# Performance work log

Hardware: AMD Instinct MI355X
Metric: run time of the kernel (lower is better)

Reference implementation:

```python
import jax, jax.numpy as jnp
import numpy as np

H = 32          # total heads
K = 8           # active heads per token
D = 128         # head_dim = embed_dim // active_heads
E = 1024        # embed_dim
S = 1024        # seq_len
MAX_SEQ = 8192
BASE = 10000.0
SCALE = D ** -0.5
LB_W = 0.01
ENT_W = 0.01


def _rope(v, cos, sin):
    # v: (T, D); cos/sin: (T, D)
    v1, v2 = v[:, : D // 2], v[:, D // 2:]
    rot = jnp.concatenate([-v2, v1], axis=-1)
    return v * cos + rot * sin


def setup_inputs() -> dict:
    key = jax.random.key(0)
    ks = jax.random.split(key, 6)
    x = jax.random.normal(ks[0], (1, S, E), jnp.float32)
    Wq = jax.random.normal(ks[1], (E, H * D), jnp.float32) * 0.02
    Wk = jax.random.normal(ks[2], (E, H * D), jnp.float32) * 0.02
    Wv = jax.random.normal(ks[3], (E, H * D), jnp.float32) * 0.02
    Wr = jax.random.normal(ks[4], (E, H), jnp.float32) * 0.02
    Wo = jax.random.normal(ks[5], (K * D, E), jnp.float32) * 0.02
    head_counts = jnp.zeros((1, H), jnp.int32)
    return {"x": x, "Wq": Wq, "Wk": Wk, "Wv": Wv, "Wr": Wr, "Wo": Wo,
            "head_counts": head_counts}


def reference(x, Wq, Wk, Wv, Wr, Wo, head_counts):
    # ---- routing (eval mode: no gumbel noise) ----
    logits = x @ Wr                                   # (1, S, H)
    soft_probs = jax.nn.softmax(logits, axis=-1)
    top_logits, head_idx = jax.lax.top_k(logits, K)   # (1, S, K)
    head_w = jax.nn.softmax(top_logits, axis=-1)      # (1, S, K)

    # ---- aux loss ----
    primary = head_idx[..., 0]                        # (1, S)
    one_hot_p = jax.nn.one_hot(primary, H, dtype=jnp.float32)
    f = one_hot_p.mean(axis=1)                        # (1, H)
    p = soft_probs.mean(axis=1)                       # (1, H)
    balance = H * (f * p).sum(axis=-1).mean()
    entropy = -(soft_probs * jnp.log(soft_probs + 1e-8)).sum(axis=-1)
    entropy_loss = -entropy.mean()
    z_loss = (jax.nn.logsumexp(logits, axis=-1) ** 2).mean() * 0.01
    aux_loss = LB_W * balance + ENT_W * entropy_loss + z_loss

    # ---- projections + per-token gather of selected heads ----
    q_all = (x @ Wq).reshape(1, S, H, D)
    k_all = (x @ Wk).reshape(1, S, H, D)
    v_all = (x @ Wv).reshape(1, S, H, D)
    gidx = head_idx[..., None]                        # (1, S, K, 1)
    q = jnp.take_along_axis(q_all, gidx, axis=2)[0].reshape(S * K, D)
    k = jnp.take_along_axis(k_all, gidx, axis=2)[0].reshape(S * K, D)
    v = jnp.take_along_axis(v_all, gidx, axis=2)[0].reshape(S * K, D)

    heads_flat = head_idx[0].reshape(S * K)           # (T,)

    # rank of each dispatched token within its head (exclusive prefix count)
    oh = jax.nn.one_hot(heads_flat, H, dtype=jnp.int32)   # (T, H)
    excl = jnp.cumsum(oh, axis=0) - oh
    rank = jnp.take_along_axis(excl, heads_flat[:, None], axis=1)[:, 0]
    positions = rank + head_counts[0, heads_flat]
    positions = jnp.clip(positions, 0, MAX_SEQ - 1)

    # ---- per-head RoPE with per-head position counters ----
    inv_freq = 1.0 / (BASE ** (jnp.arange(0, D, 2, dtype=jnp.float32) / D))
    freqs = positions.astype(jnp.float32)[:, None] * inv_freq[None, :]
    emb = jnp.concatenate([freqs, freqs], axis=-1)    # (T, D)
    cos, sin = jnp.cos(emb), jnp.sin(emb)
    q = _rope(q, cos, sin)
    k = _rope(k, cos, sin)

    # ---- block-diagonal-causal attention (same head, earlier dispatch order) ----
    idx = jnp.arange(S * K)
    mask = (heads_flat[:, None] == heads_flat[None, :]) & (idx[None, :] <= idx[:, None])
    scores = (q @ k.T) * SCALE                        # (T, T)
    scores = jnp.where(mask, scores, jnp.float32(-1e30))
    attn = jax.nn.softmax(scores, axis=-1)
    out = attn @ v                                    # (T, D)

    # ---- combine with routing weights + output projection ----
    out = out.reshape(S, K, D) * head_w[0][..., None]
    out = out.reshape(S, K * D) @ Wo                  # (S, E)
    output = out[None]                                # (1, S, E)

    updated_counts = head_counts + oh.sum(axis=0)[None]
    return output, updated_counts, aux_loss
```

## Files before the change

kernel.cpp:

```cpp
#include <hip/hip_runtime.h>
#include <math.h>

#define S 1024
#define E 1024
#define H 32
#define KSEL 8
#define D 128
#define HD 4096
#define SK 8192
#define MAXL 1024
#define CAP 9216
#define ATTN_SCALE 0.08838834764831845f
#define SSTR 36
#define PSTR 40

#define NROUTERB 1024
#define NCONV 832
#define NTAB 512

typedef _Float16 half8 __attribute__((ext_vector_type(8)));
typedef _Float16 half4 __attribute__((ext_vector_type(4)));
typedef float floatx16 __attribute__((ext_vector_type(16)));
typedef float f4 __attribute__((ext_vector_type(4)));

#define GLOAD_LDS16(gsrc, ldst) \
    __builtin_amdgcn_global_load_lds( \
        (const __attribute__((address_space(1))) void*)(gsrc), \
        (__attribute__((address_space(3))) void*)(ldst), 16, 0, 0)

__device__ __forceinline__ void head_prefix(const int* __restrict__ hlen, int h,
                                            int lane, int& len, int& hb, int& lenp)
{
    int hl = (lane < 32) ? hlen[lane] : 0;
    int hp = (hl + 31) & ~31;
    int pref = hp;
    #pragma unroll
    for (int off = 1; off < 32; off <<= 1) {
        int t = __shfl_up(pref, off, 64);
        if (lane >= off) pref += t;
    }
    int excl = pref - hp;
    hb   = __shfl(excl, h, 64);
    len  = __shfl(hl, h, 64);
    lenp = (len + 31) & ~31;
}

__global__ __launch_bounds__(256) void router_conv_kernel(
    const float* __restrict__ x, const float* __restrict__ Wr,
    int* __restrict__ head_idx, float* __restrict__ head_w,
    float* __restrict__ pbuf, float* __restrict__ entz,
    _Float16* __restrict__ xh,
    const float* __restrict__ Wq, const float* __restrict__ Wk,
    const float* __restrict__ Wv, const float* __restrict__ Wo,
    _Float16* __restrict__ Wqkt, _Float16* __restrict__ Wot,
    float2* __restrict__ tab)
{
    int bid = blockIdx.x, tid = threadIdx.x;
    __shared__ __align__(16) char smem[128 * 128 * 2];
    if (bid >= NROUTERB + NCONV) {
        int base = (bid - NROUTERB - NCONV) * 1024;
        #pragma unroll
        for (int j = 0; j < 4; ++j) {
            int idx = base + j * 256 + tid;
            int p = idx >> 6, d2 = idx & 63;
            float inv = exp2f((float)d2 * -0.20762050f);
            float ang = (float)p * inv;
            float sn, cs;
            sincosf(ang, &sn, &cs);
            tab[idx] = make_float2(cs, sn);
        }
        return;
    }
    if (bid >= NROUTERB) {
        _Float16* tl = (_Float16*)smem;
        int cb = bid - NROUTERB;
        int z, rem;
        if (cb < 768) { z = cb >> 8; rem = cb & 255; }
        else          { z = 3;       rem = cb - 768; }
        const float* W = (z == 0) ? Wq : (z == 1) ? Wk : (z == 2) ? Wv : Wo;
        _Float16* T = (z < 3) ? (Wqkt + (size_t)z * HD * E) : Wot;
        int C = (z < 3) ? HD : 1024;
        int nc = C >> 7;
        int c0 = (rem % nc) * 128;
        int r0 = (rem / nc) * 128;
        #pragma unroll
        for (int p = 0; p < 16; ++p) {
            int idx = p * 256 + tid;
            int rr = idx >> 5, cg = (idx & 31) * 4;
            f4 v = *(const f4*)&W[(size_t)(r0 + rr) * C + c0 + cg];
            half4 o;
            o.x = (_Float16)v.x; o.y = (_Float16)v.y;
            o.z = (_Float16)v.z; o.w = (_Float16)v.w;
            int sc = cg ^ (((rr >> 3) & 7) << 2);
            *(half4*)&tl[rr * 128 + sc] = o;
        }
        __syncthreads();
        #pragma unroll
        for (int p = 0; p < 8; ++p) {
            int chunk = p * 256 + tid;
            int cc = chunk >> 4, ch = chunk & 15;
            int cidx = cc ^ ((ch & 7) << 2);
            half8 o;
            #pragma unroll
            for (int j = 0; j < 8; ++j)
                o[j] = tl[(ch * 8 + j) * 128 + cidx];
            *(half8*)&T[(size_t)(c0 + cc) * 1024 + r0 + ch * 8] = o;
        }
        return;
    }
    int s = bid;
    int w = tid >> 6, lane = tid & 63;
    int h = lane & 31;
    int seg = w * 2 + (lane >> 5);
    float* partial = (float*)smem;
    const float* xr = x + (size_t)s * E + seg * 128;
    const float* wr = Wr + (size_t)(seg * 128) * H + h;
    float a0 = 0.f, a1 = 0.f, a2 = 0.f, a3 = 0.f;
    #pragma unroll 4
    for (int e = 0; e < 128; e += 4) {
        a0 += xr[e]     * wr[e * H];
        a1 += xr[e + 1] * wr[(e + 1) * H];
        a2 += xr[e + 2] * wr[(e + 2) * H];
        a3 += xr[e + 3] * wr[(e + 3) * H];
    }
    float acc = (a0 + a1) + (a2 + a3);
    acc += __shfl_xor(acc, 32, 64);
    if (lane < 32) partial[w * 32 + h] = acc;
    __syncthreads();
    float logit = partial[h] + partial[32 + h] + partial[64 + h] + partial[96 + h];
    if (w == 0) {
        float m = logit;
        #pragma unroll
        for (int off = 16; off; off >>= 1) m = fmaxf(m, __shfl_xor(m, off, 64));
        float ex = expf(logit - m);
        float Z = ex;
        #pragma unroll
        for (int off = 16; off; off >>= 1) Z += __shfl_xor(Z, off, 64);
        float p = ex / Z;
        float es = p * logf(p + 1e-8f);
        #pragma unroll
        for (int off = 16; off; off >>= 1) es += __shfl_xor(es, off, 64);
        float lse = m + logf(Z);
        float lv = logit;
        float tv[KSEL]; int ti[KSEL];
        #pragma unroll
        for (int j = 0; j < KSEL; ++j) {
            float bv = lv; int bi = h;
            #pragma unroll
            for (int off = 16; off; off >>= 1) {
                float ov = __shfl_xor(bv, off, 64);
                int oi = __shfl_xor(bi, off, 64);
                if (ov > bv || (ov == bv && oi < bi)) { bv = ov; bi = oi; }
            }
            tv[j] = bv; ti[j] = bi;
            if (h == bi) lv = -INFINITY;
        }
        float Z2 = 0.f;
        #pragma unroll
        for (int j = 0; j < KSEL; ++j) Z2 += expf(tv[j] - tv[0]);
        if (lane < 32) pbuf[s * 32 + lane] = p;
        if (lane == 0) {
            entz[s * 2]     = es;
            entz[s * 2 + 1] = lse * lse;
            #pragma unroll
            for (int j = 0; j < KSEL; ++j) {
                head_idx[s * KSEL + j] = ti[j];
                head_w[s * KSEL + j]   = expf(tv[j] - tv[0]) / Z2;
            }
        }
    }
    {
        int e = tid * 4;
        f4 v = *(const f4*)&x[(size_t)s * E + e];
        half4 o;
        o.x = (_Float16)v.x; o.y = (_Float16)v.y; o.z = (_Float16)v.z; o.w = (_Float16)v.w;
        *(half4*)&xh[(size_t)s * E + e] = o;
    }
}

__global__ __launch_bounds__(256) void scan_aux_kernel(
    const int* __restrict__ head_idx, const int* __restrict__ head_counts,
    int* __restrict__ order, int* __restrict__ hlen, float* __restrict__ out_counts,
    const float* __restrict__ pbuf, const float* __restrict__ entz,
    float* __restrict__ out_aux)
{
    int bid = blockIdx.x, tid = threadIdx.x;
    if (bid == H) {
        int hh = tid & 31, grp = tid >> 5;
        __shared__ float red[256], red2[256];
        __shared__ float psum[32];
        __shared__ int hist[32];
        if (tid < 32) hist[tid] = 0;
        float ps = 0.f;
        for (int s = grp; s < S; s += 8) ps += pbuf[s * 32 + hh];
        red[tid] = ps;
        float es = 0.f, zs = 0.f;
        for (int s = tid; s < S; s += 256) { es += entz[s * 2]; zs += entz[s * 2 + 1]; }
        red2[tid] = es;
        __syncthreads();
        if (grp == 0) {
            float v = 0.f;
            #pragma unroll
            for (int j = 0; j < 8; ++j) v += red[j * 32 + hh];
            psum[hh] = v;
        }
        __syncthreads();
        red[tid] = zs;
        for (int s = tid; s < S; s += 256)
            atomicAdd(&hist[head_idx[s * KSEL]], 1);
        __syncthreads();
        for (int stp = 128; stp; stp >>= 1) {
            if (tid < stp) { red[tid] += red[tid + stp]; red2[tid] += red2[tid + stp]; }
            __syncthreads();
        }
        if (tid == 0) {
            float bal = 0.f;
            for (int j = 0; j < H; ++j)
                bal += ((float)hist[j] / (float)S) * (psum[j] / (float)S);
            bal *= (float)H;
            float ent_loss = red2[0] / (float)S;
            float z = red[0] / (float)S * 0.01f;
            out_aux[0] = 0.01f * bal + 0.01f * ent_loss + z;
        }
        return;
    }
    int h = bid;
    int wave = tid >> 6, lane = tid & 63;
    __shared__ int wtot[4][4];
    int base = 0;
    int hc = head_counts[h];
    int v0 = head_idx[tid],       v1 = head_idx[256 + tid];
    int v2 = head_idx[512 + tid], v3 = head_idx[768 + tid];
    unsigned long long lt = (1ull << lane) - 1ull;
    for (int c0 = 0; c0 < SK; c0 += 1024) {
        int n0 = 0, n1 = 0, n2 = 0, n3 = 0;
        if (c0 + 1024 < SK) {
            n0 = head_idx[c0 + 1024 + tid]; n1 = head_idx[c0 + 1280 + tid];
            n2 = head_idx[c0 + 1536 + tid]; n3 = head_idx[c0 + 1792 + tid];
        }
        bool p0 = (v0 == h), p1 = (v1 == h), p2 = (v2 == h), p3 = (v3 == h);
        unsigned long long m0 = __ballot(p0), m1 = __ballot(p1);
        unsigned long long m2 = __ballot(p2), m3 = __ballot(p3);
        int w0 = __popcll(m0 & lt), w1 = __popcll(m1 & lt);
        int w2 = __popcll(m2 & lt), w3 = __popcll(m3 & lt);
        if (lane == 0) {
            wtot[0][wave] = __popcll(m0); wtot[1][wave] = __popcll(m1);
            wtot[2][wave] = __popcll(m2); wtot[3][wave] = __popcll(m3);
        }
        __syncthreads();
        int pw[4], T[4];
        #pragma unroll
        for (int i = 0; i < 4; ++i) {
            int pre = 0, tot = 0;
            #pragma unroll
            for (int w = 0; w < 4; ++w) {
                int tv = wtot[i][w];
                if (w < wave) pre += tv;
                tot += tv;
            }
            pw[i] = pre; T[i] = tot;
        }
        if (p0) order[h * MAXL + base + pw[0] + w0] = c0 + tid;
        if (p1) order[h * MAXL + base + T[0] + pw[1] + w1] = c0 + 256 + tid;
        if (p2) order[h * MAXL + base + T[0] + T[1] + pw[2] + w2] = c0 + 512 + tid;
        if (p3) order[h * MAXL + base + T[0] + T[1] + T[2] + pw[3] + w3] = c0 + 768 + tid;
        base += T[0] + T[1] + T[2] + T[3];
        __syncthreads();
        v0 = n0; v1 = n1; v2 = n2; v3 = n3;
    }
    if (tid == 0) {
        hlen[h] = base;
        out_counts[h] = (float)(hc + base);
    }
}

__global__ __launch_bounds__(256) void qkv_mfma(
    const _Float16* __restrict__ xh, const _Float16* __restrict__ Wt,
    const int* __restrict__ order, const int* __restrict__ hlen,
    const int* __restrict__ head_counts, const float2* __restrict__ tab,
    _Float16* __restrict__ qh, _Float16* __restrict__ kh, _Float16* __restrict__ vT)
{
    int xid = blockIdx.x;
    int qkv = xid >> 5, h = xid & 31;
    int rt = blockIdx.y;
    int tid = threadIdx.x, wave = tid >> 6, lane = tid & 63;
    int len, hb, lenp;
    head_prefix(hlen, h, lane, len, hb, lenp);
    int row0 = rt * 64;
    if (row0 >= len) return;
    int wm = wave >> 1, wn = wave & 1;
    int l32 = lane & 31, g = lane >> 5;

    __shared__ _Float16 Bs[2][128 * 64];

    int arow_g = row0 + wm * 32 + l32;
    int tok = (arow_g < len) ? (order[h * MAXL + arow_g] >> 3) : 0;
    const _Float16* aptr = xh + (size_t)tok * E;
    const _Float16* Wb = Wt + (size_t)((qkv * H + h) * D) * E;

    auto stageB = [&](int buf, int k0) {
        #pragma unroll
        for (int it = 0; it < 4; ++it) {
            int f = it * 256 + tid;
            int row = f >> 3, c = f & 7;
            int sc = c ^ (row & 7);
            const _Float16* src = Wb + (size_t)row * E + k0 + sc * 8;
            GLOAD_LDS16(src, &Bs[buf][f * 8]);
        }
    };

    floatx16 acc[2] = {};
    half8 a_cur[4], a_nxt[4];
    #pragma unroll
    for (int ks = 0; ks < 4; ++ks)
        a_cur[ks] = *(const half8*)(aptr + ks * 16 + g * 8);

    auto compute = [&](int buf, half8* a) {
        #pragma unroll
        for (int ks = 0; ks < 4; ++ks) {
            int wchunk = ks * 2 + g;
            #pragma unroll
            for (int nf = 0; nf < 2; ++nf) {
                int brow = wn * 64 + nf * 32 + l32;
                half8 bf = *(const half8*)&Bs[buf][brow * 64 + (wchunk ^ (brow & 7)) * 8];
                acc[nf] = __builtin_amdgcn_mfma_f32_32x32x16_f16(a[ks], bf, acc[nf], 0, 0, 0);
            }
        }
    };

    stageB(0, 0);
    __syncthreads();
    int buf = 0;
    for (int k0 = 64; k0 < E; k0 += 64) {
        stageB(buf ^ 1, k0);
        #pragma unroll
        for (int ks = 0; ks < 4; ++ks)
            a_nxt[ks] = *(const half8*)(aptr + k0 + ks * 16 + g * 8);
        compute(buf, a_cur);
        __syncthreads();
        buf ^= 1;
        #pragma unroll
        for (int ks = 0; ks < 4; ++ks) a_cur[ks] = a_nxt[ks];
    }
    compute(buf, a_cur);

    if (qkv < 2) {
        _Float16* dst = (qkv == 0) ? qh : kh;
        float* scr = (float*)&Bs[0][0];
        __syncthreads();
        #pragma unroll
        for (int nf = 0; nf < 2; ++nf) {
            int col = wn * 64 + nf * 32 + l32;
            #pragma unroll
            for (int reg = 0; reg < 16; ++reg) {
                int rl = wm * 32 + (reg & 3) + 8 * (reg >> 2) + 4 * g;
                scr[rl * 128 + col] = acc[nf][reg];
            }
        }
        __syncthreads();
        int hc = head_counts[h];
        #pragma unroll
        for (int pass = 0; pass < 16; ++pass) {
            int idx = pass * 256 + tid;
            int r = idx >> 6, d2 = idx & 63;
            int slot = row0 + r;
            if (slot < len) {
                float v1 = scr[r * 128 + d2], v2 = scr[r * 128 + 64 + d2];
                int p = slot + hc;
                p = p < 0 ? 0 : (p > 8191 ? 8191 : p);
                float2 tt = tab[p * 64 + d2];
                _Float16* dp = dst + ((size_t)hb + slot) * D;
                dp[d2]      = (_Float16)(v1 * tt.x - v2 * tt.y);
                dp[d2 + 64] = (_Float16)(v2 * tt.x + v1 * tt.y);
            }
        }
    } else {
        #pragma unroll
        for (int nf = 0; nf < 2; ++nf) {
            int col = wn * 64 + nf * 32 + l32;
            #pragma unroll
            for (int q4 = 0; q4 < 4; ++q4) {
                int slot0 = row0 + wm * 32 + 8 * q4 + 4 * g;
                _Float16* vp = vT + (size_t)hb * D + (size_t)col * lenp + slot0;
                if (slot0 + 3 < len) {
                    half4 o;
                    o.x = (_Float16)acc[nf][q4 * 4 + 0];
                    o.y = (_Float16)acc[nf][q4 * 4 + 1];
                    o.z = (_Float16)acc[nf][q4 * 4 + 2];
                    o.w = (_Float16)acc[nf][q4 * 4 + 3];
                    *(half4*)vp = o;
                } else {
                    #pragma unroll
                    for (int r2 = 0; r2 < 4; ++r2) {
                        int sl = slot0 + r2;
                        if (sl < len) vp[r2] = (_Float16)acc[nf][q4 * 4 + r2];
                        else if (sl < lenp) vp[r2] = (_Float16)0.f;
                    }
                }
            }
        }
    }
}

__global__ __launch_bounds__(128) void attn_mfma(
    const _Float16* __restrict__ qh, const _Float16* __restrict__ kh,
    const _Float16* __restrict__ vT,
    const int* __restrict__ order, const int* __restrict__ hlen,
    const float* __restrict__ head_w, _Float16* __restrict__ ao)
{
    int h = blockIdx.x >> 5, qt = blockIdx.x & 31;
    int tid = threadIdx.x;
    int w = tid >> 6, lane = tid & 63;
    int len, hb, lenp;
    head_prefix(hlen, h, lane, len, hb, lenp);
    int row0 = qt * 32;
    if (row0 >= len) return;
    int l32 = lane & 31, g = lane >> 5;
    int srow = lane >> 1, shalf = lane & 1;

    __shared__ float Sld[2][32 * SSTR];
    __shared__ _Float16 Pld[2][32 * PSTR];
    __shared__ float alphaLd[2][32];
    __shared__ float mlLd[32][4];
    __shared__ float facLd[32][3];
    __shared__ int flatLd[32];
    __shared__ float Obuf[32][128];

    if (tid < 32) {
        int r = row0 + tid;
        flatLd[tid] = (r < len) ? order[h * MAXL + r] : -1;
    }

    const _Float16* qrow = qh + ((size_t)hb + row0 + l32) * D;
    half8 qf[8];
    #pragma unroll
    for (int t = 0; t < 8; ++t) qf[t] = *(const half8*)(qrow + t * 16 + g * 8);

    floatx16 O[4] = {};
    float m_run = -INFINITY, l_run = 0.f;

    if (w <= qt) {
        half8 kf[8], kfn[8], vv[8];
        {
            const _Float16* krow = kh + ((size_t)hb + w * 32 + l32) * D;
            #pragma unroll
            for (int t = 0; t < 8; ++t) kf[t] = *(const half8*)(krow + t * 16 + g * 8);
        }
        for (int kt = w; kt <= qt; kt += 2) {
            int col0 = kt * 32;
            floatx16 Sc = {};
            #pragma unroll
            for (int t = 0; t < 8; ++t)
                Sc = __builtin_amdgcn_mfma_f32_32x32x16_f16(qf[t], kf[t], Sc, 0, 0, 0);
            #pragma unroll
            for (int nt = 0; nt < 4; ++nt) {
                const _Float16* vp = vT + (size_t)hb * D + (size_t)(nt * 32 + l32) * lenp + col0;
                vv[nt * 2]     = *(const half8*)(vp + g * 8);
                vv[nt * 2 + 1] = *(const half8*)(vp + 16 + g * 8);
            }
            if (kt + 2 <= qt) {
                const _Float16* krow = kh + ((size_t)hb + col0 + 64 + l32) * D;
                #pragma unroll
                for (int t = 0; t < 8; ++t) kfn[t] = *(const half8*)(krow + t * 16 + g * 8);
            }
            bool diag = (kt == qt);
            #pragma unroll
            for (int reg = 0; reg < 16; ++reg) {
                int row = (reg & 3) + 8 * (reg >> 2) + 4 * g;
                float s = Sc[reg] * ATTN_SCALE;
                if (diag && l32 > row) s = -1e30f;
                Sld[w][row * SSTR + l32] = s;
            }
            __builtin_amdgcn_wave_barrier();
            const float* sp = &Sld[w][srow * SSTR + shalf * 16];
            float va[16];
            *(f4*)(va)      = *(const f4*)(sp);
            *(f4*)(va + 4)  = *(const f4*)(sp + 4);
            *(f4*)(va + 8)  = *(const f4*)(sp + 8);
            *(f4*)(va + 12) = *(const f4*)(sp + 12);
            float mt_ = va[0];
            #pragma unroll
            for (int j = 1; j < 16; ++j) mt_ = fmaxf(mt_, va[j]);
            mt_ = fmaxf(mt_, __shfl_xor(mt_, 1, 64));
            float m_new = fmaxf(m_run, mt_);
            float alpha = __expf(m_run - m_new);
            float p[16], tsum = 0.f;
            #pragma unroll
            for (int j = 0; j < 16; ++j) { p[j] = __expf(va[j] - m_new); tsum += p[j]; }
            tsum += __shfl_xor(tsum, 1, 64);
            l_run = l_run * alpha + tsum;
            m_run = m_new;
            half8 ph0, ph1;
            #pragma unroll
            for (int j = 0; j < 8; ++j) { ph0[j] = (_Float16)p[j]; ph1[j] = (_Float16)p[j + 8]; }
            *(half8*)&Pld[w][srow * PSTR + shalf * 16]     = ph0;
            *(half8*)&Pld[w][srow * PSTR + shalf * 16 + 8] = ph1;
            if (shalf == 0) alphaLd[w][srow] = alpha;
            __builtin_amdgcn_wave_barrier();
            f4 al[4];
            #pragma unroll
            for (int qq = 0; qq < 4; ++qq) al[qq] = *(const f4*)&alphaLd[w][4 * g + 8 * qq];
            #pragma unroll
            for (int reg = 0; reg < 16; ++reg) {
                float av = al[reg >> 2][reg & 3];
                O[0][reg] *= av; O[1][reg] *= av; O[2][reg] *= av; O[3][reg] *= av;
            }
            half8 pf0 = *(const half8*)&Pld[w][l32 * PSTR + g * 8];
            half8 pf1 = *(const half8*)&Pld[w][l32 * PSTR + 16 + g * 8];
            #pragma unroll
            for (int nt = 0; nt < 4; ++nt) {
                O[nt] = __builtin_amdgcn_mfma_f32_32x32x16_f16(pf0, vv[nt * 2],     O[nt], 0, 0, 0);
                O[nt] = __builtin_amdgcn_mfma_f32_32x32x16_f16(pf1, vv[nt * 2 + 1], O[nt], 0, 0, 0);
            }
            __builtin_amdgcn_wave_barrier();
            #pragma unroll
            for (int t = 0; t < 8; ++t) kf[t] = kfn[t];
        }
    }
    if (shalf == 0) { mlLd[srow][w * 2] = m_run; mlLd[srow][w * 2 + 1] = l_run; }
    __syncthreads();
    if (tid < 32) {
        float m0 = mlLd[tid][0], l0 = mlLd[tid][1];
        float m1 = mlLd[tid][2], l1 = mlLd[tid][3];
        float ms = fmaxf(m0, m1);
        float f0 = __expf(m0 - ms), f1 = __expf(m1 - ms);
        float lt = f0 * l0 + f1 * l1;
        int flat = flatLd[tid];
        float hw = (flat >= 0) ? head_w[flat] : 0.f;
        facLd[tid][0] = f1;
        facLd[tid][1] = hw / lt;
        facLd[tid][2] = f0;
    }
    __syncthreads();
    if (w == 1) {
        #pragma unroll
        for (int nt = 0; nt < 4; ++nt) {
            int col = nt * 32 + l32;
            #pragma unroll
            for (int reg = 0; reg < 16; ++reg) {
                int row = (reg & 3) + 8 * (reg >> 2) + 4 * g;
                Obuf[row][col] = O[nt][reg] * facLd[row][0];
            }
        }
    }
    __syncthreads();
    if (w == 0) {
        #pragma unroll
        for (int nt = 0; nt < 4; ++nt) {
            int col = nt * 32 + l32;
            #pragma unroll
            for (int reg = 0; reg < 16; ++reg) {
                int row = (reg & 3) + 8 * (reg >> 2) + 4 * g;
                int flat = flatLd[row];
                if (flat >= 0) {
                    float val = (O[nt][reg] * facLd[row][2] + Obuf[row][col]) * facLd[row][1];
                    ao[(size_t)flat * D + col] = (_Float16)val;
                }
            }
        }
    }
}

__global__ __launch_bounds__(256) void out_mfma(
    const _Float16* __restrict__ A, const _Float16* __restrict__ Bt,
    float* __restrict__ C)
{
    int n0 = blockIdx.x * 64, m0 = blockIdx.y * 64;
    int tid = threadIdx.x, wave = tid >> 6, lane = tid & 63;
    int wm = wave >> 1, wn = wave & 1;
    int l32 = lane & 31, g = lane >> 5;

    __shared__ _Float16 Bs[2][64 * 64];

    const _Float16* aptr = A + (size_t)(m0 + wm * 32 + l32) * 1024;

    auto stageB = [&](int buf, int k0) {
        #pragma unroll
        for (int it = 0; it < 2; ++it) {
            int f = it * 256 + tid;
            int row = f >> 3, c = f & 7;
            int sc = c ^ (row & 7);
            GLOAD_LDS16(Bt + (size_t)(n0 + row) * 1024 + k0 + sc * 8, &Bs[buf][f * 8]);
        }
    };

    floatx16 acc = {};
    int brow = wn * 32 + l32;
    half8 a_cur[4], a_nxt[4];
    #pragma unroll
    for (int ks = 0; ks < 4; ++ks)
        a_cur[ks] = *(const half8*)(aptr + ks * 16 + g * 8);

    auto compute = [&](int buf, half8* a) {
        #pragma unroll
        for (int ks = 0; ks < 4; ++ks) {
            int wchunk = ks * 2 + g;
            half8 bf = *(const half8*)&Bs[buf][brow * 64 + (wchunk ^ (brow & 7)) * 8];
            acc = __builtin_amdgcn_mfma_f32_32x32x16_f16(a[ks], bf, acc, 0, 0, 0);
        }
    };

    stageB(0, 0);
    __syncthreads();
    int buf = 0;
    for (int k0 = 64; k0 < 1024; k0 += 64) {
        stageB(buf ^ 1, k0);
        #pragma unroll
        for (int ks = 0; ks < 4; ++ks)
            a_nxt[ks] = *(const half8*)(aptr + k0 + ks * 16 + g * 8);
        compute(buf, a_cur);
        __syncthreads();
        buf ^= 1;
        #pragma unroll
        for (int ks = 0; ks < 4; ++ks) a_cur[ks] = a_nxt[ks];
    }
    compute(buf, a_cur);

    int col = n0 + wn * 32 + l32;
    #pragma unroll
    for (int reg = 0; reg < 16; ++reg) {
        int row = m0 + wm * 32 + (reg & 3) + 8 * (reg >> 2) + 4 * g;
        C[(size_t)row * 1024 + col] = acc[reg];
    }
}

extern "C" void kernel_launch(void* const* d_in, const int* in_sizes, int n_in,
                              void* d_out, int out_size, void* d_ws, size_t ws_size,
                              hipStream_t stream)
{
    const float* x  = (const float*)d_in[0];
    const float* Wq = (const float*)d_in[1];
    const float* Wk = (const float*)d_in[2];
    const float* Wv = (const float*)d_in[3];
    const float* Wr = (const float*)d_in[4];
    const float* Wo = (const float*)d_in[5];
    const int* head_counts = (const int*)d_in[6];
    float* out = (float*)d_out;

    float* head_w = (float*)d_ws;
    float* pbuf   = head_w + SK;
    float* entz   = pbuf + S * 32;
    int* head_idx = (int*)(entz + S * 2);
    int* order    = head_idx + SK;
    int* hlen     = order + H * MAXL;
    _Float16* xh   = (_Float16*)(hlen + 64);
    _Float16* aoh  = xh + (size_t)S * E;
    _Float16* Wqkt = aoh + (size_t)SK * D;
    _Float16* Wot  = Wqkt + (size_t)3 * HD * E;
    _Float16* qh   = Wot + (size_t)1024 * 1024;
    _Float16* kh   = qh + (size_t)CAP * D;
    _Float16* vT   = kh + (size_t)CAP * D;
    float2* tab    = (float2*)(vT + (size_t)CAP * D);

    router_conv_kernel<<<NROUTERB + NCONV + NTAB, 256, 0, stream>>>(
        x, Wr, head_idx, head_w, pbuf, entz, xh, Wq, Wk, Wv, Wo, Wqkt, Wot, tab);
    scan_aux_kernel<<<33, 256, 0, stream>>>(head_idx, head_counts, order, hlen,
                                            out + (size_t)S * E, pbuf, entz,
                                            out + (size_t)S * E + H);
    qkv_mfma<<<dim3(96, 16), 256, 0, stream>>>(xh, Wqkt, order, hlen, head_counts, tab,
                                               qh, kh, vT);
    attn_mfma<<<H * 32, 128, 0, stream>>>(qh, kh, vT, order, hlen, head_w, aoh);
    out_mfma<<<dim3(16, 16), 256, 0, stream>>>(aoh, Wot, out);
}
```

Baseline: 217.0 us.

## Fuse scan into router kernel, tile Q/K/V layouts, reverse attention tile order

Three independent changes. First, the scan/aux kernel is merged into the router/convert kernel: scan blocks spin on a global atomic counter until all router blocks have finished, which removes one kernel launch but adds a hipMemsetAsync and relies on the router blocks being scheduled before the scan blocks. Second, Q, K and V^T are written by the QKV kernel in a 32-row tiled, fragment-interleaved layout so the attention kernel's MFMA operand loads are contiguous per lane. Third, attention query tiles are issued in reverse order so the longest causal tiles start first, improving load balance.

```diff
diff --git a/kernel.cpp b/kernel.cpp
--- a/kernel.cpp
+++ b/kernel.cpp
@@ -15,6 +15,7 @@
 #define PSTR 40
 
 #define NROUTERB 1024
+#define NSCAN 33
 #define NCONV 832
 #define NTAB 512
 
@@ -27,6 +28,7 @@
     __builtin_amdgcn_global_load_lds( \
         (const __attribute__((address_space(1))) void*)(gsrc), \
         (__attribute__((address_space(3))) void*)(ldst), 16, 0, 0)
+
 
 __device__ __forceinline__ void head_prefix(const int* __restrict__ hlen, int h,
                                             int lane, int& len, int& hb, int& lenp)
@@ -53,27 +55,190 @@
     const float* __restrict__ Wq, const float* __restrict__ Wk,
     const float* __restrict__ Wv, const float* __restrict__ Wo,
     _Float16* __restrict__ Wqkt, _Float16* __restrict__ Wot,
-    float2* __restrict__ tab)
+    float2* __restrict__ tab,
+    const int* __restrict__ head_counts,
+    int* __restrict__ order, int* __restrict__ hlen,
+    float* __restrict__ out_counts, float* __restrict__ out_aux,
+    int* __restrict__ syncb)
 {
     int bid = blockIdx.x, tid = threadIdx.x;
     __shared__ __align__(16) char smem[128 * 128 * 2];
-    if (bid >= NROUTERB + NCONV) {
-        int base = (bid - NROUTERB - NCONV) * 1024;
-        #pragma unroll
-        for (int j = 0; j < 4; ++j) {
-            int idx = base + j * 256 + tid;
-            int p = idx >> 6, d2 = idx & 63;
-            float inv = exp2f((float)d2 * -0.20762050f);
-            float ang = (float)p * inv;
-            float sn, cs;
-            sincosf(ang, &sn, &cs);
-            tab[idx] = make_float2(cs, sn);
-        }
+    if (bid < NROUTERB) {
+        int s = bid;
+        int w = tid >> 6, lane = tid & 63;
+        int h = lane & 31;
+        int seg = w * 2 + (lane >> 5);
+        float* partial = (float*)smem;
+        const float* xr = x + (size_t)s * E + seg * 128;
+        const float* wr = Wr + (size_t)(seg * 128) * H + h;
+        float a0 = 0.f, a1 = 0.f, a2 = 0.f, a3 = 0.f;
+        #pragma unroll 4
+        for (int e = 0; e < 128; e += 4) {
+            a0 += xr[e]     * wr[e * H];
+            a1 += xr[e + 1] * wr[(e + 1) * H];
+            a2 += xr[e + 2] * wr[(e + 2) * H];
+            a3 += xr[e + 3] * wr[(e + 3) * H];
+        }
+        float acc = (a0 + a1) + (a2 + a3);
+        acc += __shfl_xor(acc, 32, 64);
+        if (lane < 32) partial[w * 32 + h] = acc;
+        __syncthreads();
+        float logit = partial[h] + partial[32 + h] + partial[64 + h] + partial[96 + h];
+        if (w == 0) {
+            float m = logit;
+            #pragma unroll
+            for (int off = 16; off; off >>= 1) m = fmaxf(m, __shfl_xor(m, off, 64));
+            float ex = expf(logit - m);
+            float Z = ex;
+            #pragma unroll
+            for (int off = 16; off; off >>= 1) Z += __shfl_xor(Z, off, 64);
+            float p = ex / Z;
+            float es = p * logf(p + 1e-8f);
+            #pragma unroll
+            for (int off = 16; off; off >>= 1) es += __shfl_xor(es, off, 64);
+            float lse = m + logf(Z);
+            float lv = logit;
+            float tv[KSEL]; int ti[KSEL];
+            #pragma unroll
+            for (int j = 0; j < KSEL; ++j) {
+                float bv = lv; int bi = h;
+                #pragma unroll
+                for (int off = 16; off; off >>= 1) {
+                    float ov = __shfl_xor(bv, off, 64);
+                    int oi = __shfl_xor(bi, off, 64);
+                    if (ov > bv || (ov == bv && oi < bi)) { bv = ov; bi = oi; }
+                }
+                tv[j] = bv; ti[j] = bi;
+                if (h == bi) lv = -INFINITY;
+            }
+            float Z2 = 0.f;
+            #pragma unroll
+            for (int j = 0; j < KSEL; ++j) Z2 += expf(tv[j] - tv[0]);
+            if (lane < 32) pbuf[s * 32 + lane] = p;
+            if (lane == 0) {
+                entz[s * 2]     = es;
+                entz[s * 2 + 1] = lse * lse;
+                #pragma unroll
+                for (int j = 0; j < KSEL; ++j) {
+                    head_idx[s * KSEL + j] = ti[j];
+                    head_w[s * KSEL + j]   = expf(tv[j] - tv[0]) / Z2;
+                }
+            }
+        }
+        {
+            int e = tid * 4;
+            f4 v = *(const f4*)&x[(size_t)s * E + e];
+            half4 o;
+            o.x = (_Float16)v.x; o.y = (_Float16)v.y; o.z = (_Float16)v.z; o.w = (_Float16)v.w;
+            *(half4*)&xh[(size_t)s * E + e] = o;
+        }
+        __threadfence();
+        __syncthreads();
+        if (tid == 0)
+            __hip_atomic_fetch_add(&syncb[0], 1, __ATOMIC_RELEASE, __HIP_MEMORY_SCOPE_AGENT);
         return;
     }
-    if (bid >= NROUTERB) {
+    if (bid < NROUTERB + NSCAN) {
+        if (tid == 0) {
+            while (__hip_atomic_load(&syncb[0], __ATOMIC_ACQUIRE, __HIP_MEMORY_SCOPE_AGENT) < NROUTERB)
+                __builtin_amdgcn_s_sleep(8);
+        }
+        __syncthreads();
+        (void)__hip_atomic_load(&syncb[0], __ATOMIC_ACQUIRE, __HIP_MEMORY_SCOPE_AGENT);
+        int sb = bid - NROUTERB;
+        if (sb == H) {
+            float* red  = (float*)smem;
+            float* red2 = red + 256;
+            float* psum = red2 + 256;
+            int*   hist = (int*)(psum + 32);
+            int hh = tid & 31, grp = tid >> 5;
+            if (tid < 32) hist[tid] = 0;
+            float ps = 0.f;
+            for (int s = grp; s < S; s += 8) ps += pbuf[s * 32 + hh];
+            red[tid] = ps;
+            float es = 0.f, zs = 0.f;
+            for (int s = tid; s < S; s += 256) { es += entz[s * 2]; zs += entz[s * 2 + 1]; }
+            red2[tid] = es;
+            __syncthreads();
+            if (grp == 0) {
+                float v = 0.f;
+                #pragma unroll
+                for (int j = 0; j < 8; ++j) v += red[j * 32 + hh];
+                psum[hh] = v;
+            }
+            __syncthreads();
+            red[tid] = zs;
+            for (int s = tid; s < S; s += 256)
+                atomicAdd(&hist[head_idx[s * KSEL]], 1);
+            __syncthreads();
+            for (int stp = 128; stp; stp >>= 1) {
+                if (tid < stp) { red[tid] += red[tid + stp]; red2[tid] += red2[tid + stp]; }
+                __syncthreads();
+            }
+            if (tid == 0) {
+                float bal = 0.f;
+                for (int j = 0; j < H; ++j)
+                    bal += ((float)hist[j] / (float)S) * (psum[j] / (float)S);
+                bal *= (float)H;
+                float ent_loss = red2[0] / (float)S;
+                float z = red[0] / (float)S * 0.01f;
+                out_aux[0] = 0.01f * bal + 0.01f * ent_loss + z;
+            }
+            return;
+        }
+        int h = sb;
+        int wave = tid >> 6, lane = tid & 63;
+        int (*wtot)[4] = (int(*)[4])smem;
+        int base = 0;
+        int hc = head_counts[h];
+        int v0 = head_idx[tid],       v1 = head_idx[256 + tid];
+        int v2 = head_idx[512 + tid], v3 = head_idx[768 + tid];
+        unsigned long long lt = (1ull << lane) - 1ull;
+        for (int c0 = 0; c0 < SK; c0 += 1024) {
+            int n0 = 0, n1 = 0, n2 = 0, n3 = 0;
+            if (c0 + 1024 < SK) {
+                n0 = head_idx[c0 + 1024 + tid]; n1 = head_idx[c0 + 1280 + tid];
+                n2 = head_idx[c0 + 1536 + tid]; n3 = head_idx[c0 + 1792 + tid];
+            }
+            bool p0 = (v0 == h), p1 = (v1 == h), p2 = (v2 == h), p3 = (v3 == h);
+            unsigned long long m0 = __ballot(p0), m1 = __ballot(p1);
+            unsigned long long m2 = __ballot(p2), m3 = __ballot(p3);
+            int w0 = __popcll(m0 & lt), w1 = __popcll(m1 & lt);
+            int w2 = __popcll(m2 & lt), w3 = __popcll(m3 & lt);
+            if (lane == 0) {
+                wtot[0][wave] = __popcll(m0); wtot[1][wave] = __popcll(m1);
+                wtot[2][wave] = __popcll(m2); wtot[3][wave] = __popcll(m3);
+            }
+            __syncthreads();
+            int pw[4], T[4];
+            #pragma unroll
+            for (int i = 0; i < 4; ++i) {
+                int pre = 0, tot = 0;
+                #pragma unroll
+                for (int w = 0; w < 4; ++w) {
+                    int tv = wtot[i][w];
+                    if (w < wave) pre += tv;
+                    tot += tv;
+                }
+                pw[i] = pre; T[i] = tot;
+            }
+            if (p0) order[h * MAXL + base + pw[0] + w0] = c0 + tid;
+            if (p1) order[h * MAXL + base + T[0] + pw[1] + w1] = c0 + 256 + tid;
+            if (p2) order[h * MAXL + base + T[0] + T[1] + pw[2] + w2] = c0 + 512 + tid;
+            if (p3) order[h * MAXL + base + T[0] + T[1] + T[2] + pw[3] + w3] = c0 + 768 + tid;
+            base += T[0] + T[1] + T[2] + T[3];
+            __syncthreads();
+            v0 = n0; v1 = n1; v2 = n2; v3 = n3;
+        }
+        if (tid == 0) {
+            hlen[h] = base;
+            out_counts[h] = (float)(hc + base);
+        }
+        return;
+    }
+    if (bid < NROUTERB + NSCAN + NCONV) {
         _Float16* tl = (_Float16*)smem;
-        int cb = bid - NROUTERB;
+        int cb = bid - NROUTERB - NSCAN;
         int z, rem;
         if (cb < 768) { z = cb >> 8; rem = cb & 255; }
         else          { z = 3;       rem = cb - 768; }
@@ -108,169 +273,16 @@
         }
         return;
     }
-    int s = bid;
-    int w = tid >> 6, lane = tid & 63;
-    int h = lane & 31;
-    int seg = w * 2 + (lane >> 5);
-    float* partial = (float*)smem;
-    const float* xr = x + (size_t)s * E + seg * 128;
-    const float* wr = Wr + (size_t)(seg * 128) * H + h;
-    float a0 = 0.f, a1 = 0.f, a2 = 0.f, a3 = 0.f;
-    #pragma unroll 4
-    for (int e = 0; e < 128; e += 4) {
-        a0 += xr[e]     * wr[e * H];
-        a1 += xr[e + 1] * wr[(e + 1) * H];
-        a2 += xr[e + 2] * wr[(e + 2) * H];
-        a3 += xr[e + 3] * wr[(e + 3) * H];
-    }
-    float acc = (a0 + a1) + (a2 + a3);
-    acc += __shfl_xor(acc, 32, 64);
-    if (lane < 32) partial[w * 32 + h] = acc;
-    __syncthreads();
-    float logit = partial[h] + partial[32 + h] + partial[64 + h] + partial[96 + h];
-    if (w == 0) {
-        float m = logit;
-        #pragma unroll
-        for (int off = 16; off; off >>= 1) m = fmaxf(m, __shfl_xor(m, off, 64));
-        float ex = expf(logit - m);
-        float Z = ex;
-        #pragma unroll
-        for (int off = 16; off; off >>= 1) Z += __shfl_xor(Z, off, 64);
-        float p = ex / Z;
-        float es = p * logf(p + 1e-8f);
-        #pragma unroll
-        for (int off = 16; off; off >>= 1) es += __shfl_xor(es, off, 64);
-        float lse = m + logf(Z);
-        float lv = logit;
-        float tv[KSEL]; int ti[KSEL];
-        #pragma unroll
-        for (int j = 0; j < KSEL; ++j) {
-            float bv = lv; int bi = h;
-            #pragma unroll
-            for (int off = 16; off; off >>= 1) {
-                float ov = __shfl_xor(bv, off, 64);
-                int oi = __shfl_xor(bi, off, 64);
-                if (ov > bv || (ov == bv && oi < bi)) { bv = ov; bi = oi; }
-            }
-            tv[j] = bv; ti[j] = bi;
-            if (h == bi) lv = -INFINITY;
-        }
-        float Z2 = 0.f;
-        #pragma unroll
-        for (int j = 0; j < KSEL; ++j) Z2 += expf(tv[j] - tv[0]);
-        if (lane < 32) pbuf[s * 32 + lane] = p;
-        if (lane == 0) {
-            entz[s * 2]     = es;
-            entz[s * 2 + 1] = lse * lse;
-            #pragma unroll
-            for (int j = 0; j < KSEL; ++j) {
-                head_idx[s * KSEL + j] = ti[j];
-                head_w[s * KSEL + j]   = expf(tv[j] - tv[0]) / Z2;
-            }
-        }
-    }
-    {
-        int e = tid * 4;
-        f4 v = *(const f4*)&x[(size_t)s * E + e];
-        half4 o;
-        o.x = (_Float16)v.x; o.y = (_Float16)v.y; o.z = (_Float16)v.z; o.w = (_Float16)v.w;
-        *(half4*)&xh[(size_t)s * E + e] = o;
-    }
-}
-
-__global__ __launch_bounds__(256) void scan_aux_kernel(
-    const int* __restrict__ head_idx, const int* __restrict__ head_counts,
-    int* __restrict__ order, int* __restrict__ hlen, float* __restrict__ out_counts,
-    const float* __restrict__ pbuf, const float* __restrict__ entz,
-    float* __restrict__ out_aux)
-{
-    int bid = blockIdx.x, tid = threadIdx.x;
-    if (bid == H) {
-        int hh = tid & 31, grp = tid >> 5;
-        __shared__ float red[256], red2[256];
-        __shared__ float psum[32];
-        __shared__ int hist[32];
-        if (tid < 32) hist[tid] = 0;
-        float ps = 0.f;
-        for (int s = grp; s < S; s += 8) ps += pbuf[s * 32 + hh];
-        red[tid] = ps;
-        float es = 0.f, zs = 0.f;
-        for (int s = tid; s < S; s += 256) { es += entz[s * 2]; zs += entz[s * 2 + 1]; }
-        red2[tid] = es;
-        __syncthreads();
-        if (grp == 0) {
-            float v = 0.f;
-            #pragma unroll
-            for (int j = 0; j < 8; ++j) v += red[j * 32 + hh];
-            psum[hh] = v;
-        }
-        __syncthreads();
-        red[tid] = zs;
-        for (int s = tid; s < S; s += 256)
-            atomicAdd(&hist[head_idx[s * KSEL]], 1);
-        __syncthreads();
-        for (int stp = 128; stp; stp >>= 1) {
-            if (tid < stp) { red[tid] += red[tid + stp]; red2[tid] += red2[tid + stp]; }
-            __syncthreads();
-        }
-        if (tid == 0) {
-            float bal = 0.f;
-            for (int j = 0; j < H; ++j)
-                bal += ((float)hist[j] / (float)S) * (psum[j] / (float)S);
-            bal *= (float)H;
-            float ent_loss = red2[0] / (float)S;
-            float z = red[0] / (float)S * 0.01f;
-            out_aux[0] = 0.01f * bal + 0.01f * ent_loss + z;
-        }
-        return;
-    }
-    int h = bid;
-    int wave = tid >> 6, lane = tid & 63;
-    __shared__ int wtot[4][4];
-    int base = 0;
-    int hc = head_counts[h];
-    int v0 = head_idx[tid],       v1 = head_idx[256 + tid];
-    int v2 = head_idx[512 + tid], v3 = head_idx[768 + tid];
-    unsigned long long lt = (1ull << lane) - 1ull;
-    for (int c0 = 0; c0 < SK; c0 += 1024) {
-        int n0 = 0, n1 = 0, n2 = 0, n3 = 0;
-        if (c0 + 1024 < SK) {
-            n0 = head_idx[c0 + 1024 + tid]; n1 = head_idx[c0 + 1280 + tid];
-            n2 = head_idx[c0 + 1536 + tid]; n3 = head_idx[c0 + 1792 + tid];
-        }
-        bool p0 = (v0 == h), p1 = (v1 == h), p2 = (v2 == h), p3 = (v3 == h);
-        unsigned long long m0 = __ballot(p0), m1 = __ballot(p1);
-        unsigned long long m2 = __ballot(p2), m3 = __ballot(p3);
-        int w0 = __popcll(m0 & lt), w1 = __popcll(m1 & lt);
-        int w2 = __popcll(m2 & lt), w3 = __popcll(m3 & lt);
-        if (lane == 0) {
-            wtot[0][wave] = __popcll(m0); wtot[1][wave] = __popcll(m1);
-            wtot[2][wave] = __popcll(m2); wtot[3][wave] = __popcll(m3);
-        }
-        __syncthreads();
-        int pw[4], T[4];
-        #pragma unroll
-        for (int i = 0; i < 4; ++i) {
-            int pre = 0, tot = 0;
-            #pragma unroll
-            for (int w = 0; w < 4; ++w) {
-                int tv = wtot[i][w];
-                if (w < wave) pre += tv;
-                tot += tv;
-            }
-            pw[i] = pre; T[i] = tot;
-        }
-        if (p0) order[h * MAXL + base + pw[0] + w0] = c0 + tid;
-        if (p1) order[h * MAXL + base + T[0] + pw[1] + w1] = c0 + 256 + tid;
-        if (p2) order[h * MAXL + base + T[0] + T[1] + pw[2] + w2] = c0 + 512 + tid;
-        if (p3) order[h * MAXL + base + T[0] + T[1] + T[2] + pw[3] + w3] = c0 + 768 + tid;
-        base += T[0] + T[1] + T[2] + T[3];
-        __syncthreads();
-        v0 = n0; v1 = n1; v2 = n2; v3 = n3;
-    }
-    if (tid == 0) {
-        hlen[h] = base;
-        out_counts[h] = (float)(hc + base);
+    int base = (bid - NROUTERB - NSCAN - NCONV) * 1024;
+    #pragma unroll
+    for (int j = 0; j < 4; ++j) {
+        int idx = base + j * 256 + tid;
+        int p = idx >> 6, d2 = idx & 63;
+        float inv = exp2f((float)d2 * -0.20762050f);
+        float ang = (float)p * inv;
+        float sn, cs;
+        sincosf(ang, &sn, &cs);
+        tab[idx] = make_float2(cs, sn);
     }
 }
 
@@ -369,9 +381,11 @@
                 int p = slot + hc;
                 p = p < 0 ? 0 : (p > 8191 ? 8191 : p);
                 float2 tt = tab[p * 64 + d2];
-                _Float16* dp = dst + ((size_t)hb + slot) * D;
-                dp[d2]      = (_Float16)(v1 * tt.x - v2 * tt.y);
-                dp[d2 + 64] = (_Float16)(v2 * tt.x + v1 * tt.y);
+                size_t tb = (size_t)(hb + (slot & ~31)) * D;
+                int sl5 = slot & 31;
+                int c0 = d2 >> 3, e0 = d2 & 7;
+                dst[tb + (size_t)(c0 * 32 + sl5) * 8 + e0]       = (_Float16)(v1 * tt.x - v2 * tt.y);
+                dst[tb + (size_t)((c0 + 8) * 32 + sl5) * 8 + e0] = (_Float16)(v2 * tt.x + v1 * tt.y);
             }
         }
     } else {
@@ -381,7 +395,9 @@
             #pragma unroll
             for (int q4 = 0; q4 < 4; ++q4) {
                 int slot0 = row0 + wm * 32 + 8 * q4 + 4 * g;
-                _Float16* vp = vT + (size_t)hb * D + (size_t)col * lenp + slot0;
+                size_t tb = (size_t)(hb + (slot0 & ~31)) * D;
+                int sc = (slot0 & 31) >> 3;
+                _Float16* vp = vT + tb + (size_t)(sc * 128 + col) * 8 + (slot0 & 7);
                 if (slot0 + 3 < len) {
                     half4 o;
                     o.x = (_Float16)acc[nf][q4 * 4 + 0];
@@ -408,7 +424,8 @@
     const int* __restrict__ order, const int* __restrict__ hlen,
     const float* __restrict__ head_w, _Float16* __restrict__ ao)
 {
-    int h = blockIdx.x >> 5, qt = blockIdx.x & 31;
+    int h = blockIdx.x >> 5;
+    int qt = 31 - (int)(blockIdx.x & 31);
     int tid = threadIdx.x;
     int w = tid >> 6, lane = tid & 63;
     int len, hb, lenp;
@@ -431,10 +448,11 @@
         flatLd[tid] = (r < len) ? order[h * MAXL + r] : -1;
     }
 
-    const _Float16* qrow = qh + ((size_t)hb + row0 + l32) * D;
+    const _Float16* qtile = qh + (size_t)(hb + row0) * D;
     half8 qf[8];
     #pragma unroll
-    for (int t = 0; t < 8; ++t) qf[t] = *(const half8*)(qrow + t * 16 + g * 8);
+    for (int t = 0; t < 8; ++t)
+        qf[t] = *(const half8*)(qtile + (size_t)((t * 2 + g) * 32 + l32) * 8);
 
     floatx16 O[4] = {};
     float m_run = -INFINITY, l_run = 0.f;
@@ -442,9 +460,10 @@
     if (w <= qt) {
         half8 kf[8], kfn[8], vv[8];
         {
-            const _Float16* krow = kh + ((size_t)hb + w * 32 + l32) * D;
-            #pragma unroll
-            for (int t = 0; t < 8; ++t) kf[t] = *(const half8*)(krow + t * 16 + g * 8);
+            const _Float16* ktile = kh + (size_t)(hb + w * 32) * D;
+            #pragma unroll
+            for (int t = 0; t < 8; ++t)
+                kf[t] = *(const half8*)(ktile + (size_t)((t * 2 + g) * 32 + l32) * 8);
         }
         for (int kt = w; kt <= qt; kt += 2) {
             int col0 = kt * 32;
@@ -452,16 +471,19 @@
             #pragma unroll
             for (int t = 0; t < 8; ++t)
                 Sc = __builtin_amdgcn_mfma_f32_32x32x16_f16(qf[t], kf[t], Sc, 0, 0, 0);
-            #pragma unroll
-            for (int nt = 0; nt < 4; ++nt) {
-                const _Float16* vp = vT + (size_t)hb * D + (size_t)(nt * 32 + l32) * lenp + col0;
-                vv[nt * 2]     = *(const half8*)(vp + g * 8);
-                vv[nt * 2 + 1] = *(const half8*)(vp + 16 + g * 8);
+            {
+                const _Float16* vtile = vT + (size_t)(hb + col0) * D;
+                #pragma unroll
+                for (int nt = 0; nt < 4; ++nt) {
+                    vv[nt * 2]     = *(const half8*)(vtile + (size_t)(g * 128 + nt * 32 + l32) * 8);
+                    vv[nt * 2 + 1] = *(const half8*)(vtile + (size_t)((2 + g) * 128 + nt * 32 + l32) * 8);
+                }
             }
             if (kt + 2 <= qt) {
-                const _Float16* krow = kh + ((size_t)hb + col0 + 64 + l32) * D;
+                const _Float16* ktile = kh + (size_t)(hb + col0 + 64) * D;
                 #pragma unroll
-                for (int t = 0; t < 8; ++t) kfn[t] = *(const half8*)(krow + t * 16 + g * 8);
+                for (int t = 0; t < 8; ++t)
+                    kfn[t] = *(const half8*)(ktile + (size_t)((t * 2 + g) * 32 + l32) * 8);
             }
             bool diag = (kt == qt);
             #pragma unroll
@@ -651,12 +673,12 @@
     _Float16* kh   = qh + (size_t)CAP * D;
     _Float16* vT   = kh + (size_t)CAP * D;
     float2* tab    = (float2*)(vT + (size_t)CAP * D);
-
-    router_conv_kernel<<<NROUTERB + NCONV + NTAB, 256, 0, stream>>>(
-        x, Wr, head_idx, head_w, pbuf, entz, xh, Wq, Wk, Wv, Wo, Wqkt, Wot, tab);
-    scan_aux_kernel<<<33, 256, 0, stream>>>(head_idx, head_counts, order, hlen,
-                                            out + (size_t)S * E, pbuf, entz,
-                                            out + (size_t)S * E + H);
+    int* syncb     = (int*)(tab + (size_t)8192 * 64);
+
+    hipMemsetAsync(syncb, 0, 16, stream);
+    router_conv_kernel<<<NROUTERB + NSCAN + NCONV + NTAB, 256, 0, stream>>>(
+        x, Wr, head_idx, head_w, pbuf, entz, xh, Wq, Wk, Wv, Wo, Wqkt, Wot, tab,
+        head_counts, order, hlen, out + (size_t)S * E, out + (size_t)S * E + H, syncb);
     qkv_mfma<<<dim3(96, 16), 256, 0, stream>>>(xh, Wqkt, order, hlen, head_counts, tab,
                                                qh, kh, vT);
     attn_mfma<<<H * 32, 128, 0, stream>>>(qh, kh, vT, order, hlen, head_w, aoh);
```

Result: slower. 369.5 us (+70.3%).
